# Performance work log

Measured on AMD Instinct MI355X. Metric: run time of the kernel, lower is better.

## Reference

```python
import jax, jax.numpy as jnp
import numpy as np

B, T, H, A = 64, 512, 1024, 256  # T == max_sen_len by construction of attention_u
PAD_VAL = -2.0 ** 22


def setup_inputs() -> dict:
    key = jax.random.key(0)
    k1, k2, k3, k4 = jax.random.split(key, 4)
    inputs = jax.random.normal(k1, (B, T, H), dtype=jnp.float32)
    sen_len = jax.random.randint(k2, (B,), 1, T + 1, dtype=jnp.int32)
    W = jax.random.normal(k3, (H, A), dtype=jnp.float32) * (1.0 / np.sqrt(H))
    b = jnp.zeros((A,), dtype=jnp.float32)
    U = jax.random.normal(k4, (A, T), dtype=jnp.float32) * (1.0 / np.sqrt(A))
    return {"inputs": inputs, "sen_len": sen_len, "W": W, "b": b, "U": U}


def reference(inputs, sen_len, W, b, U):
    # Dense with tanh: [B,T,H] @ [H,A] -> [B,T,A]
    alpha = jnp.tanh(jnp.einsum('bth,ha->bta', inputs, W) + b)
    # Score against attention_u: [B,T,A] @ [A,T] -> [B,T,T]
    scores = jnp.einsum('bta,as->bts', alpha, U)
    # sequence mask over last (key) dim, broadcast over query dim
    mask = jnp.arange(T)[None, :] < sen_len[:, None]        # [B,T]
    scores = jnp.where(mask[:, None, :], scores, jnp.float32(PAD_VAL))
    p = jax.nn.softmax(scores, axis=-1)                     # [B,T,T]
    # Weighted sum pooling: [B,T,T] @ [B,T,H] -> [B,T,H]
    Z = jnp.einsum('bts,bsh->bth', p, inputs)
    # dropout: is_training=False -> identity
    return Z
```

## Files before the change

kernel.cpp:

```cpp
#include <hip/hip_runtime.h>
#include <hip/hip_bf16.h>

typedef short short8 __attribute__((ext_vector_type(8)));
typedef short short4v __attribute__((ext_vector_type(4)));
typedef float f32x4 __attribute__((ext_vector_type(4)));
typedef __bf16 bf16x8 __attribute__((ext_vector_type(8)));

template <int ROWS>
__device__ __forceinline__ void stage2(const __hip_bfloat16* __restrict__ g,
                                       int ld, short* lds, int t) {
    const int w = t >> 6;
    const int lane = t & 63;
#pragma unroll
    for (int i = 0; i < ROWS / 64; ++i) {
        const int cb = i * 512 + w * 64;
        const int c = cb + lane;
        const int row = c >> 3;
        const int kc = (c & 7) ^ (row & 7);
        __builtin_amdgcn_global_load_lds((const void*)(g + (long)row * ld + kc * 8),
                                         (void*)(lds + cb * 8), 16, 0, 0);
    }
}

__global__ __launch_bounds__(512, 4) void gemm_xw_kernel(
    const float* __restrict__ Xf,
    const __hip_bfloat16* __restrict__ Wt,
    __hip_bfloat16* __restrict__ alpha,
    const float* __restrict__ bias) {
    __shared__ __align__(16) short smB[3][8192];
    __shared__ __align__(16) short smA[2][8192];

    int bx = blockIdx.x, by = blockIdx.y;
    {
        const int nx = gridDim.x, ny = gridDim.y;
        const int nwg = nx * ny;
        const int lin = bx + nx * by;
        const int swz = (lin & 7) * (nwg >> 3) + (lin >> 3);
        bx = swz % nx;
        by = swz / nx;
    }

    const int t = threadIdx.x;
    const int w = t >> 6, lane = t & 63;
    const int wm = w >> 1, wn = w & 1;
    const int fr = lane & 15, quad = lane >> 4;

    const float* Ab = Xf + (long)by * 128 * 1024;
    const __hip_bfloat16* Bb = Wt + (long)bx * 128 * 1024;

    int acs[2], arow[2], akc[2];
#pragma unroll
    for (int i = 0; i < 2; ++i) {
        acs[i] = i * 512 + t;
        arow[i] = acs[i] >> 3;
        akc[i] = ((acs[i] & 7) ^ (arow[i] & 7)) * 8;
    }

    f32x4 acc[2][4] = {};
    float4 rAs[2][2][2];

#define XW_ISSUE_B(KT, BUF) stage2<128>(Bb + (KT) * 64, 1024, &smB[BUF][0], t);

#define XW_LOAD_A(KT, S)                                                        \
    _Pragma("unroll") for (int i = 0; i < 2; ++i) {                             \
        const float* src = Ab + (long)arow[i] * 1024 + (KT) * 64 + akc[i];      \
        rAs[S][i][0] = *(const float4*)(src);                                   \
        rAs[S][i][1] = *(const float4*)(src + 4);                               \
    }

#define XW_WRITE_A(BUF, S)                                                      \
    _Pragma("unroll") for (int i = 0; i < 2; ++i) {                             \
        __hip_bfloat16 tmp[8] __attribute__((aligned(16)));                     \
        tmp[0] = __float2bfloat16(rAs[S][i][0].x);                              \
        tmp[1] = __float2bfloat16(rAs[S][i][0].y);                              \
        tmp[2] = __float2bfloat16(rAs[S][i][0].z);                              \
        tmp[3] = __float2bfloat16(rAs[S][i][0].w);                              \
        tmp[4] = __float2bfloat16(rAs[S][i][1].x);                              \
        tmp[5] = __float2bfloat16(rAs[S][i][1].y);                              \
        tmp[6] = __float2bfloat16(rAs[S][i][1].z);                              \
        tmp[7] = __float2bfloat16(rAs[S][i][1].w);                              \
        *(short8*)(void*)&smA[BUF][acs[i] * 8] = *(short8*)(void*)tmp;          \
    }

    XW_LOAD_A(0, 0)
    XW_ISSUE_B(0, 0)
    XW_ISSUE_B(1, 1)
    XW_WRITE_A(0, 0)
    XW_LOAD_A(1, 1)
    XW_LOAD_A(2, 0)
    __builtin_amdgcn_sched_barrier(0);
    asm volatile("s_waitcnt vmcnt(10)" ::: "memory");
    asm volatile("s_waitcnt lgkmcnt(0)" ::: "memory");
    __builtin_amdgcn_s_barrier();
    __builtin_amdgcn_sched_barrier(0);

#define XW_STEP(K)                                                              \
    {                                                                           \
        if ((K) + 2 < 16) { XW_ISSUE_B((K) + 2, ((K) + 2) % 3) }                \
        const short* At_ = &smA[(K) % 2][0];                                    \
        const short* Bt_ = &smB[(K) % 3][0];                                    \
        _Pragma("unroll") for (int ks = 0; ks < 2; ++ks) {                      \
            bf16x8 af[2], bfv[4];                                               \
            const int kc = ks * 4 + quad;                                       \
            _Pragma("unroll") for (int m = 0; m < 2; ++m) {                     \
                const int row = wm * 32 + m * 16 + fr;                          \
                const int chunk = row * 8 + (kc ^ (row & 7));                   \
                af[m] = *(const bf16x8*)(const void*)(At_ + chunk * 8);         \
            }                                                                   \
            _Pragma("unroll") for (int n = 0; n < 4; ++n) {                     \
                const int row = wn * 64 + n * 16 + fr;                          \
                const int chunk = row * 8 + (kc ^ (row & 7));                   \
                bfv[n] = *(const bf16x8*)(const void*)(Bt_ + chunk * 8);        \
            }                                                                   \
            _Pragma("unroll") for (int m = 0; m < 2; ++m)                       \
                _Pragma("unroll") for (int n = 0; n < 4; ++n)                   \
                    acc[m][n] = __builtin_amdgcn_mfma_f32_16x16x32_bf16(        \
                        af[m], bfv[n], acc[m][n], 0, 0, 0);                     \
        }                                                                       \
        if ((K) + 1 < 16) { XW_WRITE_A(((K) + 1) % 2, ((K) + 1) & 1) }          \
        if ((K) + 3 < 16) { XW_LOAD_A((K) + 3, ((K) + 1) & 1) }                 \
        __builtin_amdgcn_sched_barrier(0);                                      \
        if ((K) + 3 < 16) {                                                     \
            asm volatile("s_waitcnt vmcnt(10)" ::: "memory");                   \
        } else if ((K) + 2 < 16) {                                              \
            asm volatile("s_waitcnt vmcnt(6)" ::: "memory");                    \
        } else if ((K) + 1 < 16) {                                              \
            asm volatile("s_waitcnt vmcnt(0)" ::: "memory");                    \
        }                                                                       \
        if ((K) + 1 < 16) {                                                     \
            asm volatile("s_waitcnt lgkmcnt(0)" ::: "memory");                  \
            __builtin_amdgcn_s_barrier();                                       \
            __builtin_amdgcn_sched_barrier(0);                                  \
        }                                                                       \
    }

    XW_STEP(0)  XW_STEP(1)  XW_STEP(2)  XW_STEP(3)
    XW_STEP(4)  XW_STEP(5)  XW_STEP(6)  XW_STEP(7)
    XW_STEP(8)  XW_STEP(9)  XW_STEP(10) XW_STEP(11)
    XW_STEP(12) XW_STEP(13) XW_STEP(14) XW_STEP(15)
#undef XW_STEP
#undef XW_ISSUE_B
#undef XW_LOAD_A
#undef XW_WRITE_A

    const long rowBase = (long)by * 128 + wm * 32;
    const int colBase = bx * 128 + wn * 64;
#pragma unroll
    for (int m = 0; m < 2; ++m) {
#pragma unroll
        for (int n = 0; n < 4; ++n) {
            const int col = colBase + n * 16 + fr;
            const float bv = bias[col];
#pragma unroll
            for (int j = 0; j < 4; ++j) {
                const long row = rowBase + m * 16 + quad * 4 + j;
                alpha[row * 256 + col] = __float2bfloat16(tanhf(acc[m][n][j] + bv));
            }
        }
    }
}

__global__ __launch_bounds__(512, 4) void gemm_pv_kernel(
    const __hip_bfloat16* __restrict__ P,
    const float* __restrict__ Xf,
    float* __restrict__ Z) {
    __shared__ __align__(16) short smA[3][8192];
    __shared__ __align__(16) short smB[2][5120];

    int bx = blockIdx.x, by = blockIdx.y, bz = blockIdx.z;
    {
        const int nx = gridDim.x, ny = gridDim.y;
        const int nwg = nx * ny * gridDim.z;
        const int lin = bx + nx * (by + ny * bz);
        const int swz = (lin & 7) * (nwg >> 3) + (lin >> 3);
        bx = swz % nx;
        const int r = swz / nx;
        by = r % ny;
        bz = r / ny;
    }

    const int t = threadIdx.x;
    const int w = t >> 6, lane = t & 63;
    const int wm = w >> 1, wn = w & 1;
    const int fr = lane & 15, quad = lane >> 4;

    const __hip_bfloat16* Ab = P + ((long)bz * 512 + by * 256) * 512;
    const float* Bb = Xf + (long)bz * 512 * 1024 + bx * 128;

    int acb[2], arow[2], akc[2];
#pragma unroll
    for (int i = 0; i < 2; ++i) {
        acb[i] = i * 512 + w * 64;
        const int s = acb[i] + lane;
        arow[i] = s >> 2;
        akc[i] = ((s & 3) ^ ((arow[i] >> 1) & 3)) * 8;
    }
    const int bi = t & 15;
    const int bhc = t >> 4;

    f32x4 acc[4][4] = {};
    float4 r0s[2], r1s[2];

#define PV_ISSUE_A(KT, BUF)                                                     \
    _Pragma("unroll") for (int i = 0; i < 2; ++i)                               \
        __builtin_amdgcn_global_load_lds(                                       \
            (const void*)(Ab + (long)arow[i] * 512 + (KT) * 32 + akc[i]),       \
            (void*)(&smA[BUF][acb[i] * 8]), 16, 0, 0);

#define PV_LOAD_B(KT, S)                                                        \
    {                                                                           \
        const float* s0 = Bb + (long)((KT) * 32 + 2 * bi) * 1024 + bhc * 4;     \
        r0s[S] = *(const float4*)(s0);                                          \
        r1s[S] = *(const float4*)(s0 + 1024);                                   \
    }

#define PV_WRITE_B(BUF, S)                                                      \
    {                                                                           \
        int* dst = (int*)(void*)&smB[BUF][(bhc * 4) * 40 + bi * 2];             \
        _Pragma("unroll") for (int j = 0; j < 4; ++j) {                         \
            __hip_bfloat16 h0 = __float2bfloat16(((const float*)&r0s[S])[j]);   \
            __hip_bfloat16 h1 = __float2bfloat16(((const float*)&r1s[S])[j]);   \
            dst[j * 20] = (int)*(unsigned short*)&h0 |                          \
                          ((int)*(unsigned short*)&h1 << 16);                   \
        }                                                                       \
    }

    PV_ISSUE_A(0, 0)
    PV_ISSUE_A(1, 1)
    PV_LOAD_B(0, 0)
    PV_WRITE_B(0, 0)
    PV_LOAD_B(1, 1)
    PV_LOAD_B(2, 0)
    __builtin_amdgcn_sched_barrier(0);
    asm volatile("s_waitcnt vmcnt(6)" ::: "memory");
    asm volatile("s_waitcnt lgkmcnt(0)" ::: "memory");
    __builtin_amdgcn_s_barrier();
    __builtin_amdgcn_sched_barrier(0);

#define PV_STEP(K)                                                              \
    {                                                                           \
        if ((K) + 2 < 16) { PV_ISSUE_A((K) + 2, ((K) + 2) % 3) }                \
        const short* At_ = &smA[(K) % 3][0];                                    \
        const short* Bt_ = &smB[(K) % 2][0];                                    \
        bf16x8 bfv[4];                                                          \
        _Pragma("unroll") for (int n = 0; n < 4; ++n) {                         \
            const int h = wn * 64 + n * 16 + fr;                                \
            bfv[n] = *(const bf16x8*)(const void*)(Bt_ + h * 40 + quad * 8);    \
        }                                                                       \
        _Pragma("unroll") for (int m = 0; m < 4; ++m) {                         \
            const int row = wm * 64 + m * 16 + fr;                              \
            const int slot = row * 4 + (quad ^ ((row >> 1) & 3));               \
            const bf16x8 af = *(const bf16x8*)(const void*)(At_ + slot * 8);    \
            _Pragma("unroll") for (int n = 0; n < 4; ++n)                       \
                acc[m][n] = __builtin_amdgcn_mfma_f32_16x16x32_bf16(            \
                    af, bfv[n], acc[m][n], 0, 0, 0);                            \
        }                                                                       \
        if ((K) + 1 < 16) { PV_WRITE_B(((K) + 1) % 2, ((K) + 1) & 1) }          \
        if ((K) + 3 < 16) { PV_LOAD_B((K) + 3, ((K) + 1) & 1) }                 \
        __builtin_amdgcn_sched_barrier(0);                                      \
        if ((K) + 3 < 16) {                                                     \
            asm volatile("s_waitcnt vmcnt(6)" ::: "memory");                    \
        } else if ((K) + 2 < 16) {                                              \
            asm volatile("s_waitcnt vmcnt(4)" ::: "memory");                    \
        } else if ((K) + 1 < 16) {                                              \
            asm volatile("s_waitcnt vmcnt(0)" ::: "memory");                    \
        }                                                                       \
        if ((K) + 1 < 16) {                                                     \
            asm volatile("s_waitcnt lgkmcnt(0)" ::: "memory");                  \
            __builtin_amdgcn_s_barrier();                                       \
            __builtin_amdgcn_sched_barrier(0);                                  \
        }                                                                       \
    }

    PV_STEP(0)  PV_STEP(1)  PV_STEP(2)  PV_STEP(3)
    PV_STEP(4)  PV_STEP(5)  PV_STEP(6)  PV_STEP(7)
    PV_STEP(8)  PV_STEP(9)  PV_STEP(10) PV_STEP(11)
    PV_STEP(12) PV_STEP(13) PV_STEP(14) PV_STEP(15)
#undef PV_STEP
#undef PV_ISSUE_A
#undef PV_LOAD_B
#undef PV_WRITE_B

    const long rowBase = (long)bz * 512 + by * 256 + wm * 64;
    const int colBase = bx * 128 + wn * 64;
#pragma unroll
    for (int m = 0; m < 4; ++m) {
#pragma unroll
        for (int n = 0; n < 4; ++n) {
            const int col = colBase + n * 16 + fr;
#pragma unroll
            for (int j = 0; j < 4; ++j) {
                const long row = rowBase + m * 16 + quad * 4 + j;
                Z[row * 1024 + col] = acc[m][n][j];
            }
        }
    }
}

__global__ __launch_bounds__(256) void transpose_cvt_kernel(const float* __restrict__ in,
                                                            __hip_bfloat16* __restrict__ out,
                                                            int R, int C) {
    const int o = blockIdx.x * 256 + threadIdx.x;
    if (o >= R * C) return;
    const int c = o / R;
    const int r = o - c * R;
    out[o] = __float2bfloat16(in[(long)r * C + c]);
}

__global__ __launch_bounds__(512, 4) void score_softmax_kernel(
    const __hip_bfloat16* __restrict__ Aa,
    const __hip_bfloat16* __restrict__ Ut,
    __hip_bfloat16* __restrict__ P,
    const int* __restrict__ sen) {
    __shared__ __align__(16) short At[2048 * 8];
    __shared__ float red[2][64][9];

    const int t = threadIdx.x;
    const int w = t >> 6, lane = t & 63;
    const int fr = lane & 15, quad = lane >> 4;
    const long row0 = (long)blockIdx.x * 64;
    const __hip_bfloat16* Ab = Aa + row0 * 256;

#pragma unroll
    for (int i = 0; i < 4; ++i) {
        const int cb = i * 512 + w * 64;
        const int c = cb + lane;
        const int row = c >> 5;
        const int kc = (c & 31) ^ (row & 7);
        __builtin_amdgcn_global_load_lds(
            (const void*)(Ab + (long)row * 256 + kc * 8),
            (void*)(At + cb * 8), 16, 0, 0);
    }

    f32x4 acc[4][4] = {};
    bf16x8 bfvs[2][4];

#define SM_LOAD_B(KT, S)                                                        \
    _Pragma("unroll") for (int n = 0; n < 4; ++n)                               \
        bfvs[S][n] = *(const bf16x8*)(const void*)(                             \
            Ut + (w * 64 + n * 16 + fr) * 256 + (KT) * 32 + quad * 8);

    SM_LOAD_B(0, 0)
    SM_LOAD_B(1, 1)
    __builtin_amdgcn_sched_barrier(0);
    asm volatile("s_waitcnt vmcnt(8)" ::: "memory");
    __builtin_amdgcn_s_barrier();
    __builtin_amdgcn_sched_barrier(0);

#define SM_STEP(KT)                                                             \
    {                                                                           \
        bf16x8 af[4];                                                           \
        _Pragma("unroll") for (int m = 0; m < 4; ++m) {                         \
            const int row = m * 16 + fr;                                        \
            const int g = row * 32 + (((KT) * 4 + quad) ^ (row & 7));           \
            af[m] = *(const bf16x8*)(const void*)(At + g * 8);                  \
        }                                                                       \
        _Pragma("unroll") for (int m = 0; m < 4; ++m)                           \
            _Pragma("unroll") for (int n = 0; n < 4; ++n)                       \
                acc[m][n] = __builtin_amdgcn_mfma_f32_16x16x32_bf16(            \
                    af[m], bfvs[(KT) & 1][n], acc[m][n], 0, 0, 0);              \
        if ((KT) + 2 < 8) { SM_LOAD_B((KT) + 2, (KT) & 1) }                     \
    }

    SM_STEP(0) SM_STEP(1) SM_STEP(2) SM_STEP(3)
    SM_STEP(4) SM_STEP(5) SM_STEP(6) SM_STEP(7)
#undef SM_STEP
#undef SM_LOAD_B
    __syncthreads();

    const int L = sen[row0 >> 9];
    bool valid[4];
#pragma unroll
    for (int n = 0; n < 4; ++n) valid[n] = (w * 64 + n * 16 + fr) < L;

    float mx[4][4];
#pragma unroll
    for (int m = 0; m < 4; ++m)
#pragma unroll
        for (int j = 0; j < 4; ++j) {
            float v = -3.0e38f;
#pragma unroll
            for (int n = 0; n < 4; ++n)
                if (valid[n]) v = fmaxf(v, acc[m][n][j]);
#pragma unroll
            for (int off = 8; off >= 1; off >>= 1) v = fmaxf(v, __shfl_xor(v, off, 64));
            mx[m][j] = v;
        }
    if (fr == 0) {
#pragma unroll
        for (int m = 0; m < 4; ++m)
#pragma unroll
            for (int j = 0; j < 4; ++j) red[0][m * 16 + quad * 4 + j][w] = mx[m][j];
    }
    __syncthreads();
    float rmax[4][4];
#pragma unroll
    for (int m = 0; m < 4; ++m)
#pragma unroll
        for (int j = 0; j < 4; ++j) {
            const int row = m * 16 + quad * 4 + j;
            float v = red[0][row][0];
#pragma unroll
            for (int ww = 1; ww < 8; ++ww) v = fmaxf(v, red[0][row][ww]);
            rmax[m][j] = v;
        }

    float sum[4][4];
#pragma unroll
    for (int m = 0; m < 4; ++m)
#pragma unroll
        for (int j = 0; j < 4; ++j) {
            float s = 0.f;
#pragma unroll
            for (int n = 0; n < 4; ++n) {
                float e = valid[n] ? __expf(acc[m][n][j] - rmax[m][j]) : 0.f;
                acc[m][n][j] = e;
                s += e;
            }
#pragma unroll
            for (int off = 8; off >= 1; off >>= 1) s += __shfl_xor(s, off, 64);
            sum[m][j] = s;
        }
    if (fr == 0) {
#pragma unroll
        for (int m = 0; m < 4; ++m)
#pragma unroll
            for (int j = 0; j < 4; ++j) red[1][m * 16 + quad * 4 + j][w] = sum[m][j];
    }
    __syncthreads();
#pragma unroll
    for (int m = 0; m < 4; ++m)
#pragma unroll
        for (int j = 0; j < 4; ++j) {
            const int row = m * 16 + quad * 4 + j;
            float s = 0.f;
#pragma unroll
            for (int ww = 0; ww < 8; ++ww) s += red[1][row][ww];
            const float inv = 1.f / s;
#pragma unroll
            for (int n = 0; n < 4; ++n)
                P[(row0 + row) * 512 + w * 64 + n * 16 + fr] =
                    __float2bfloat16(acc[m][n][j] * inv);
        }
}

extern "C" void kernel_launch(void* const* d_in, const int* in_sizes, int n_in,
                              void* d_out, int out_size, void* d_ws, size_t ws_size,
                              hipStream_t stream) {
    const float* X = (const float*)d_in[0];
    const int* sen = (const int*)d_in[1];
    const float* W = (const float*)d_in[2];
    const float* bias = (const float*)d_in[3];
    const float* U = (const float*)d_in[4];
    float* out = (float*)d_out;

    const int B = 64, T = 512, H = 1024, A = 256;
    const long M = (long)B * T;

    char* ws = (char*)d_ws;
    __hip_bfloat16* Pbf = (__hip_bfloat16*)ws;
    __hip_bfloat16* Wt = (__hip_bfloat16*)(ws + M * T * 2);
    __hip_bfloat16* Ut = (__hip_bfloat16*)((char*)Wt + (long)H * A * 2);

    __hip_bfloat16* alpha = (__hip_bfloat16*)((char*)d_out + M * H * 2);

    transpose_cvt_kernel<<<(H * A) / 256, 256, 0, stream>>>(W, Wt, H, A);
    transpose_cvt_kernel<<<(A * T) / 256, 256, 0, stream>>>(U, Ut, A, T);
    gemm_xw_kernel<<<dim3(2, 256), 512, 0, stream>>>(X, Wt, alpha, bias);
    score_softmax_kernel<<<(int)(M / 64), 512, 0, stream>>>(alpha, Ut, Pbf, sen);
    gemm_pv_kernel<<<dim3(H / 128, T / 256, B), 512, 0, stream>>>(Pbf, X, out);
}
```

Measured before the change: 141.7 us.

## Stream fp32 X tiles directly to LDS and convert to bf16 at fragment load

The PV GEMM's B operand (fp32 inputs) was previously loaded to registers, converted to bf16 and written to a padded LDS tile. It is now fetched with global_load_lds straight into a triple-buffered fp32 LDS tile, and bf16 conversion happens per lane when building MFMA fragments. This removes the register staging and the explicit LDS write path, and unifies A and B into one async pipeline. In exchange it doubles LDS footprint for B (lowering occupancy, launch bounds drop to 2), adds strided scalar LDS reads with possible bank conflicts, and repeats conversion work across waves.

```diff
diff --git a/kernel.cpp b/kernel.cpp
--- a/kernel.cpp
+++ b/kernel.cpp
@@ -160,12 +160,12 @@
     }
 }
 
-__global__ __launch_bounds__(512, 4) void gemm_pv_kernel(
+__global__ __launch_bounds__(512, 2) void gemm_pv_kernel(
     const __hip_bfloat16* __restrict__ P,
     const float* __restrict__ Xf,
     float* __restrict__ Z) {
     __shared__ __align__(16) short smA[3][8192];
-    __shared__ __align__(16) short smB[2][5120];
+    __shared__ __align__(16) float smB[3][4096];
 
     int bx = blockIdx.x, by = blockIdx.y, bz = blockIdx.z;
     {
@@ -195,11 +195,8 @@
         arow[i] = s >> 2;
         akc[i] = ((s & 3) ^ ((arow[i] >> 1) & 3)) * 8;
     }
-    const int bi = t & 15;
-    const int bhc = t >> 4;
 
     f32x4 acc[4][4] = {};
-    float4 r0s[2], r1s[2];
 
 #define PV_ISSUE_A(KT, BUF)                                                     \
     _Pragma("unroll") for (int i = 0; i < 2; ++i)                               \
@@ -207,45 +204,38 @@
             (const void*)(Ab + (long)arow[i] * 512 + (KT) * 32 + akc[i]),       \
             (void*)(&smA[BUF][acb[i] * 8]), 16, 0, 0);
 
-#define PV_LOAD_B(KT, S)                                                        \
-    {                                                                           \
-        const float* s0 = Bb + (long)((KT) * 32 + 2 * bi) * 1024 + bhc * 4;     \
-        r0s[S] = *(const float4*)(s0);                                          \
-        r1s[S] = *(const float4*)(s0 + 1024);                                   \
-    }
-
-#define PV_WRITE_B(BUF, S)                                                      \
-    {                                                                           \
-        int* dst = (int*)(void*)&smB[BUF][(bhc * 4) * 40 + bi * 2];             \
-        _Pragma("unroll") for (int j = 0; j < 4; ++j) {                         \
-            __hip_bfloat16 h0 = __float2bfloat16(((const float*)&r0s[S])[j]);   \
-            __hip_bfloat16 h1 = __float2bfloat16(((const float*)&r1s[S])[j]);   \
-            dst[j * 20] = (int)*(unsigned short*)&h0 |                          \
-                          ((int)*(unsigned short*)&h1 << 16);                   \
-        }                                                                       \
+#define PV_ISSUE_B(KT, BUF)                                                     \
+    _Pragma("unroll") for (int i = 0; i < 2; ++i) {                             \
+        const int g = i * 512 + t;                                              \
+        __builtin_amdgcn_global_load_lds(                                       \
+            (const void*)(Bb + (long)((KT) * 32 + (g >> 5)) * 1024 + (g & 31) * 4), \
+            (void*)(&smB[BUF][(i * 512 + w * 64) * 4]), 16, 0, 0);              \
     }
 
     PV_ISSUE_A(0, 0)
+    PV_ISSUE_B(0, 0)
     PV_ISSUE_A(1, 1)
-    PV_LOAD_B(0, 0)
-    PV_WRITE_B(0, 0)
-    PV_LOAD_B(1, 1)
-    PV_LOAD_B(2, 0)
-    __builtin_amdgcn_sched_barrier(0);
-    asm volatile("s_waitcnt vmcnt(6)" ::: "memory");
-    asm volatile("s_waitcnt lgkmcnt(0)" ::: "memory");
+    PV_ISSUE_B(1, 1)
+    __builtin_amdgcn_sched_barrier(0);
+    asm volatile("s_waitcnt vmcnt(4)" ::: "memory");
     __builtin_amdgcn_s_barrier();
     __builtin_amdgcn_sched_barrier(0);
 
 #define PV_STEP(K)                                                              \
     {                                                                           \
-        if ((K) + 2 < 16) { PV_ISSUE_A((K) + 2, ((K) + 2) % 3) }                \
+        if ((K) + 2 < 16) {                                                     \
+            PV_ISSUE_A((K) + 2, ((K) + 2) % 3)                                  \
+            PV_ISSUE_B((K) + 2, ((K) + 2) % 3)                                  \
+        }                                                                       \
         const short* At_ = &smA[(K) % 3][0];                                    \
-        const short* Bt_ = &smB[(K) % 2][0];                                    \
+        const float* Bt_ = &smB[(K) % 3][0];                                    \
         bf16x8 bfv[4];                                                          \
         _Pragma("unroll") for (int n = 0; n < 4; ++n) {                         \
-            const int h = wn * 64 + n * 16 + fr;                                \
-            bfv[n] = *(const bf16x8*)(const void*)(Bt_ + h * 40 + quad * 8);    \
+            const float* col = Bt_ + quad * 8 * 128 + wn * 64 + n * 16 + fr;    \
+            __hip_bfloat16 tmp[8] __attribute__((aligned(16)));                 \
+            _Pragma("unroll") for (int j = 0; j < 8; ++j)                       \
+                tmp[j] = __float2bfloat16(col[j * 128]);                        \
+            bfv[n] = *(bf16x8*)(void*)tmp;                                      \
         }                                                                       \
         _Pragma("unroll") for (int m = 0; m < 4; ++m) {                         \
             const int row = wm * 64 + m * 16 + fr;                              \
@@ -255,18 +245,13 @@
                 acc[m][n] = __builtin_amdgcn_mfma_f32_16x16x32_bf16(            \
                     af, bfv[n], acc[m][n], 0, 0, 0);                            \
         }                                                                       \
-        if ((K) + 1 < 16) { PV_WRITE_B(((K) + 1) % 2, ((K) + 1) & 1) }          \
-        if ((K) + 3 < 16) { PV_LOAD_B((K) + 3, ((K) + 1) & 1) }                 \
         __builtin_amdgcn_sched_barrier(0);                                      \
-        if ((K) + 3 < 16) {                                                     \
-            asm volatile("s_waitcnt vmcnt(6)" ::: "memory");                    \
-        } else if ((K) + 2 < 16) {                                              \
+        if ((K) + 2 < 16) {                                                     \
             asm volatile("s_waitcnt vmcnt(4)" ::: "memory");                    \
         } else if ((K) + 1 < 16) {                                              \
             asm volatile("s_waitcnt vmcnt(0)" ::: "memory");                    \
         }                                                                       \
         if ((K) + 1 < 16) {                                                     \
-            asm volatile("s_waitcnt lgkmcnt(0)" ::: "memory");                  \
             __builtin_amdgcn_s_barrier();                                       \
             __builtin_amdgcn_sched_barrier(0);                                  \
         }                                                                       \
@@ -278,8 +263,7 @@
     PV_STEP(12) PV_STEP(13) PV_STEP(14) PV_STEP(15)
 #undef PV_STEP
 #undef PV_ISSUE_A
-#undef PV_LOAD_B
-#undef PV_WRITE_B
+#undef PV_ISSUE_B
 
     const long rowBase = (long)bz * 512 + by * 256 + wm * 64;
     const int colBase = bx * 128 + wn * 64;
```

Result: slower. 148.2 us (+4.6%).
